# Kernel optimization log

Hardware: AMD Instinct MI355X
Metric: run time of the kernel (lower is better)

Reference implementation:

```python
import jax, jax.numpy as jnp
import numpy as np

D_MODEL = 1440; D_INNER = 2880; D_STATE = 128; HEADDIM = 64; NHEADS = 45
D_CONV = 4; NLAYERS = 32; VOCAB = 256; CHUNK = 128
D_XBC = D_INNER + 2 * D_STATE          # 3136 conv channels
D_PROJ = 2 * D_INNER + 2 * D_STATE + NHEADS  # 6061 in_proj width
EPS = 1e-5

def silu(x):
    return x * jax.nn.sigmoid(x)

def segsum(x):
    # x: (..., T) -> (..., T, T); out[i, j] = sum_{j < k <= i} x[k], -inf above diagonal
    T = x.shape[-1]
    xe = jnp.broadcast_to(x[..., None], (*x.shape, T))
    lower = jnp.tril(jnp.ones((T, T), bool), -1)
    cs = jnp.cumsum(jnp.where(lower, xe, 0.0), axis=-2)
    return jnp.where(jnp.tril(jnp.ones((T, T), bool)), cs, -jnp.inf)

def ssd(X, A, B, C):
    # Chunked SSD (Mamba2 'ssd_minimal_discrete'). X:(b,l,h,p) pre-multiplied by dt,
    # A:(b,l,h) = dt * A_head, B/C:(b,l,n) (ngroups=1, shared across heads).
    b, l, h, p = X.shape
    n = B.shape[-1]
    c = l // CHUNK
    Xc = X.reshape(b, c, CHUNK, h, p)
    Ac = A.reshape(b, c, CHUNK, h).transpose(0, 3, 1, 2)      # (b,h,c,q)
    Bc = B.reshape(b, c, CHUNK, n)
    Cc = C.reshape(b, c, CHUNK, n)
    A_cs = jnp.cumsum(Ac, axis=-1)                            # (b,h,c,q)
    L = jnp.exp(segsum(Ac))                                   # (b,h,c,q,q) intra-chunk decay
    Y_diag = jnp.einsum('bcln,bcsn,bhcls,bcshp->bclhp', Cc, Bc, L, Xc)
    decay_states = jnp.exp(A_cs[..., -1:] - A_cs)             # (b,h,c,q)
    states = jnp.einsum('bcln,bhcl,bclhp->bchpn', Bc, decay_states, Xc)
    A_last = jnp.pad(A_cs[..., -1], ((0, 0), (0, 0), (1, 0)))  # (b,h,c+1)
    decay_chunk = jnp.exp(segsum(A_last))                     # (b,h,c+1,c+1)
    states = jnp.concatenate([jnp.zeros_like(states[:, :1]), states], axis=1)
    states = jnp.einsum('bhzc,bchpn->bzhpn', decay_chunk, states)[:, :-1]  # (b,c,h,p,n)
    Y_off = jnp.einsum('bcln,bchpn,bhcl->bclhp', Cc, states, jnp.exp(A_cs))
    return (Y_diag + Y_off).reshape(b, l, h, p)

def mamba2_block(h, p):
    Win, conv_w, conv_b, dt_bias, A_log, Dp, norm_w, Wout = p
    b, l, _ = h.shape
    zxbcdt = h @ Win                                           # (b,l,6061)
    z = zxbcdt[..., :D_INNER]
    xBC = zxbcdt[..., D_INNER:D_INNER + D_XBC]
    dt = jax.nn.softplus(zxbcdt[..., -NHEADS:] + dt_bias)      # (b,l,H)
    # causal depthwise conv over time, kernel 4
    xp = jnp.pad(xBC, ((0, 0), (D_CONV - 1, 0), (0, 0))).transpose(0, 2, 1)  # (b,C,l+3)
    xBC = jax.lax.conv_general_dilated(xp, conv_w[:, None, :], (1,), 'VALID',
            feature_group_count=D_XBC, dimension_numbers=('NCH', 'OIH', 'NCH'))
    xBC = silu(xBC.transpose(0, 2, 1) + conv_b)                # (b,l,3136)
    x = xBC[..., :D_INNER].reshape(b, l, NHEADS, HEADDIM)
    B = xBC[..., D_INNER:D_INNER + D_STATE]
    C = xBC[..., D_INNER + D_STATE:]
    A = -jnp.exp(A_log)                                        # (H,)
    y = ssd(x * dt[..., None], dt * A, B, C)
    y = y + x * Dp[None, None, :, None]                        # D skip (on raw x)
    y = y.reshape(b, l, D_INNER) * silu(z)                     # gate, then RMSNormGated
    y = y * jax.lax.rsqrt(jnp.mean(y * y, -1, keepdims=True) + EPS) * norm_w
    return y @ Wout

def setup_inputs() -> dict:
    key = jax.random.key(0)
    ks = jax.random.split(key, 8)
    b, l = 2, 2048
    def nrm(k, shape, s=0.02):
        return jax.random.normal(k, shape, jnp.float32) * s
    tokens = jax.random.randint(ks[0], (b, l), 0, VOCAB)
    embed = nrm(ks[1], (VOCAB, D_MODEL))
    Win = nrm(ks[2], (NLAYERS, D_MODEL, D_PROJ))
    conv_w = nrm(ks[3], (NLAYERS, D_XBC, D_CONV), 0.2)
    conv_b = jnp.zeros((NLAYERS, D_XBC), jnp.float32)
    dtv = jnp.exp(jax.random.uniform(ks[4], (NLAYERS, NHEADS)) * (np.log(0.1) - np.log(1e-3)) + np.log(1e-3))
    dt_bias = dtv + jnp.log(-jnp.expm1(-dtv))                  # inverse softplus
    A_log = jnp.log(jax.random.uniform(ks[5], (NLAYERS, NHEADS), minval=1.0, maxval=16.0))
    Dp = jnp.ones((NLAYERS, NHEADS), jnp.float32)
    norm_w = jnp.ones((NLAYERS, D_INNER), jnp.float32)
    Wout = nrm(ks[6], (NLAYERS, D_INNER, D_MODEL))
    final_norm_w = jnp.ones((D_MODEL,), jnp.float32)
    return {'tokens': tokens, 'embed': embed, 'Win': Win, 'conv_w': conv_w,
            'conv_b': conv_b, 'dt_bias': dt_bias, 'A_log': A_log, 'Dp': Dp,
            'norm_w': norm_w, 'Wout': Wout, 'final_norm_w': final_norm_w}

def reference(tokens, embed, Win, conv_w, conv_b, dt_bias, A_log, Dp, norm_w, Wout, final_norm_w):
    h = embed[tokens]                                          # (b,l,d)
    layer_params = (Win, conv_w, conv_b, dt_bias, A_log, Dp, norm_w, Wout)
    def step(carry, p):
        return carry + mamba2_block(carry, p), None
    h, _ = jax.lax.scan(jax.checkpoint(step), h, layer_params)
    h = h * jax.lax.rsqrt(jnp.mean(h * h, -1, keepdims=True) + EPS) * final_norm_w
    return h @ embed.T                                         # tied head -> (b,l,256)
```

## Files before the change

kernel.cpp:

```cpp
#include <hip/hip_runtime.h>
#include <hip/hip_bf16.h>
#include <math.h>

#define NLAYERS 32
#define DM 1440
#define DI 2880
#define DSTATE 128
#define HD 64
#define NH 45
#define VOCABSZ 256
#define CHUNK 128
#define DXBC 3136
#define DPROJ 6061
#define BB 2
#define LL 2048
#define ROWS (BB*LL)
#define NCH (LL/CHUNK)
#define ZXS 6144
#define STR 136
#define STR2 68

typedef __attribute__((ext_vector_type(8))) short bf16x8;
typedef __attribute__((ext_vector_type(4))) float f32x4;
typedef unsigned short us;

__device__ __forceinline__ float sigmoidf_(float x){ return 1.0f/(1.0f+__expf(-x)); }
__device__ __forceinline__ us f2b(float f){
  unsigned int u = __float_as_uint(f);
  return (us)((u + 0x7FFFu + ((u>>16)&1u)) >> 16);
}
__device__ __forceinline__ float b2f(us s){
  return __uint_as_float(((unsigned int)s)<<16);
}
__device__ __forceinline__ void split2(float v, us* ph, us* pl){
  us h = f2b(v);
  *ph = h;
  *pl = f2b(v - b2f(h));
}
__device__ __forceinline__ void gl2lds16(const us* g, us* l){
  __builtin_amdgcn_global_load_lds((const __attribute__((address_space(1))) unsigned int*)g,
                                   (__attribute__((address_space(3))) unsigned int*)l, 16, 0, 0);
}
#define MFMA(a,b,c) __builtin_amdgcn_mfma_f32_16x16x32_bf16(a,b,c,0,0,0)

__global__ void k_embed(const int* __restrict__ tok, const float* __restrict__ emb, float* __restrict__ h){
  int idx = blockIdx.x*256 + threadIdx.x;
  if (idx >= ROWS*DM) return;
  int row = idx / DM, d = idx - row*DM;
  h[idx] = emb[tok[row]*DM + d];
}

__global__ void k_split_rows(const float* __restrict__ src, us* __restrict__ dh,
                             us* __restrict__ dl, int ncols){
  size_t e = ((size_t)blockIdx.x*256 + threadIdx.x)*8;
  const float* s = src + e;
  bf16x8 oh, ol;
  #pragma unroll
  for (int j=0;j<8;j++){
    float v = s[j];
    us hh = f2b(v);
    ((us*)&oh)[j] = hh;
    ((us*)&ol)[j] = f2b(v - b2f(hh));
  }
  *(bf16x8*)(dh + e) = oh;
  *(bf16x8*)(dl + e) = ol;
}

__global__ void k_transcast_sp(const float* __restrict__ W, us* __restrict__ WTh,
                               us* __restrict__ WTl, int K, int N){
  __shared__ float t[32][65];
  int tid = threadIdx.x;
  int n0 = blockIdx.x*64, k0 = blockIdx.y*32;
  #pragma unroll
  for (int i=0;i<8;i++){
    int e = i*256 + tid;
    int r = e >> 6, cc = e & 63;
    int n = n0 + cc;
    t[r][cc] = (n < N) ? W[(size_t)(k0+r)*N + n] : 0.f;
  }
  __syncthreads();
  int nrow = tid >> 2, kseg = (tid & 3)*8;
  bf16x8 oh, ol;
  #pragma unroll
  for (int j=0;j<8;j++){
    float v = t[kseg+j][nrow];
    us hh = f2b(v);
    ((us*)&oh)[j] = hh;
    ((us*)&ol)[j] = f2b(v - b2f(hh));
  }
  *(bf16x8*)(WTh + (size_t)(n0+nrow)*K + k0 + kseg) = oh;
  *(bf16x8*)(WTl + (size_t)(n0+nrow)*K + k0 + kseg) = ol;
}

template<bool ACC, bool SPL>
__global__ __launch_bounds__(256) void k_gemm_sp(const us* __restrict__ Ah, const us* __restrict__ Al,
      const us* __restrict__ Bh, const us* __restrict__ Bl, float* __restrict__ C,
      int K, int ldc, int N, int nbx, us* __restrict__ Oh, us* __restrict__ Ol){
  __shared__ __align__(16) us sAh[4096], sAl[4096], sBh[4096], sBl[4096];
  int nwg = gridDim.x;
  int q = nwg >> 3;
  int bid = blockIdx.x;
  int wg = (bid & 7)*q + (bid >> 3);
  int grp = wg / (4*nbx);
  int rem = wg - grp*4*nbx;
  int by = grp*4 + (rem & 3);
  int bx = rem >> 2;
  int m0 = by*128, n0 = bx*128;
  int tid = threadIdx.x;
  int lane = tid & 63, wid = tid >> 6;
  int wr = wid >> 1, wc = wid & 1;
  int r4 = lane >> 2, c4 = (lane & 3)*8;
  int fr = lane & 15, fk = (lane >> 4)*8;
  f32x4 acc[4][4];
  #pragma unroll
  for (int i=0;i<4;i++)
    #pragma unroll
    for (int j=0;j<4;j++) acc[i][j] = (f32x4){0.f,0.f,0.f,0.f};
  for (int kt = 0; kt < K; kt += 32){
    __syncthreads();
    size_t ra0 = (size_t)(m0 + wid*16     + r4)*K + kt + c4;
    size_t ra1 = (size_t)(m0 + (wid+4)*16 + r4)*K + kt + c4;
    size_t rb0 = (size_t)(n0 + wid*16     + r4)*K + kt + c4;
    size_t rb1 = (size_t)(n0 + (wid+4)*16 + r4)*K + kt + c4;
    gl2lds16(Ah + ra0, sAh + wid*512);
    gl2lds16(Ah + ra1, sAh + (wid+4)*512);
    gl2lds16(Al + ra0, sAl + wid*512);
    gl2lds16(Al + ra1, sAl + (wid+4)*512);
    gl2lds16(Bh + rb0, sBh + wid*512);
    gl2lds16(Bh + rb1, sBh + (wid+4)*512);
    gl2lds16(Bl + rb0, sBl + wid*512);
    gl2lds16(Bl + rb1, sBl + (wid+4)*512);
    __syncthreads();
    bf16x8 ah[4], al[4], bh[4], bl[4];
    #pragma unroll
    for (int i=0;i<4;i++){
      int ro = (wr*64 + i*16 + fr)*32 + fk;
      int co = (wc*64 + i*16 + fr)*32 + fk;
      ah[i] = *(const bf16x8*)(sAh + ro);
      al[i] = *(const bf16x8*)(sAl + ro);
      bh[i] = *(const bf16x8*)(sBh + co);
      bl[i] = *(const bf16x8*)(sBl + co);
    }
    #pragma unroll
    for (int i=0;i<4;i++)
      #pragma unroll
      for (int j=0;j<4;j++){
        acc[i][j] = MFMA(ah[i], bh[j], acc[i][j]);
        acc[i][j] = MFMA(ah[i], bl[j], acc[i][j]);
        acc[i][j] = MFMA(al[i], bh[j], acc[i][j]);
      }
  }
  int orow = (lane>>4)*4, ocol = lane & 15;
  #pragma unroll
  for (int i=0;i<4;i++)
    #pragma unroll
    for (int j=0;j<4;j++)
      #pragma unroll
      for (int r=0;r<4;r++){
        int col = n0 + wc*64 + j*16 + ocol;
        if (col < N){
          size_t off = (size_t)(m0 + wr*64 + i*16 + orow + r)*ldc + col;
          float v = acc[i][j][r] + (ACC ? C[off] : 0.f);
          C[off] = v;
          if (SPL) split2(v, &Oh[off], &Ol[off]);
        }
      }
}

__global__ __launch_bounds__(256) void k_conv2(const float* __restrict__ zx, const float* __restrict__ cw,
                        const float* __restrict__ cb, us* __restrict__ xbh, us* __restrict__ xbl,
                        const float* __restrict__ dtb_in, float* __restrict__ dtb){
  int ch = blockIdx.x*256 + threadIdx.x;
  int l0 = blockIdx.y * 128;
  int b = blockIdx.z;
  if (ch < DXBC){
    float w0 = cw[ch*4+0], w1 = cw[ch*4+1], w2 = cw[ch*4+2], w3 = cw[ch*4+3];
    float bias = cb[ch];
    float x0=0.f, x1=0.f, x2=0.f;
    if (l0-3 >= 0) x0 = zx[(size_t)(b*LL + l0-3)*ZXS + DI + ch];
    if (l0-2 >= 0) x1 = zx[(size_t)(b*LL + l0-2)*ZXS + DI + ch];
    if (l0-1 >= 0) x2 = zx[(size_t)(b*LL + l0-1)*ZXS + DI + ch];
    for (int l = l0; l < l0+128; ++l){
      float x3 = zx[(size_t)(b*LL + l)*ZXS + DI + ch];
      float s = bias + w0*x0 + w1*x1 + w2*x2 + w3*x3;
      float v = s * sigmoidf_(s);
      size_t off = (size_t)(b*LL + l)*DXBC + ch;
      split2(v, &xbh[off], &xbl[off]);
      x0 = x1; x1 = x2; x2 = x3;
    }
  } else if (ch < DXBC + NH){
    int hh = ch - DXBC;
    float bias = dtb_in[hh];
    for (int l = l0; l < l0+128; ++l){
      size_t row = (size_t)(b*LL + l);
      float v = zx[row*ZXS + (DI+DXBC) + hh] + bias;
      dtb[row*NH + hh] = (v > 20.f) ? v : log1pf(__expf(v));
    }
  }
}

__global__ __launch_bounds__(256) void k_sraw(const us* __restrict__ xbh, const us* __restrict__ xbl,
                                              float* __restrict__ Sraw){
  __shared__ __align__(16) us sCh[128*STR], sCl[128*STR], sB2h[128*STR], sB2l[128*STR];
  int tid = threadIdx.x;
  int c = blockIdx.x, b = blockIdx.y;
  int t0 = b*LL + c*CHUNK;
  #pragma unroll
  for (int i=0;i<8;i++){
    int e = i*256 + tid;
    int l = e >> 4, seg = (e & 15)*8;
    size_t oc = (size_t)(t0+l)*DXBC + DI + DSTATE + seg;
    size_t ob = (size_t)(t0+l)*DXBC + DI + seg;
    *(bf16x8*)(sCh + l*STR + seg) = *(const bf16x8*)(xbh + oc);
    *(bf16x8*)(sCl + l*STR + seg) = *(const bf16x8*)(xbl + oc);
    *(bf16x8*)(sB2h + l*STR + seg) = *(const bf16x8*)(xbh + ob);
    *(bf16x8*)(sB2l + l*STR + seg) = *(const bf16x8*)(xbl + ob);
  }
  __syncthreads();
  int lane = tid & 63, wid = tid >> 6;
  int wbase = wid*32;
  int fr = lane & 15, fk = (lane>>4)*8;
  int orow = (lane>>4)*4;
  f32x4 accS[2][8];
  #pragma unroll
  for (int m=0;m<2;m++)
    #pragma unroll
    for (int j=0;j<8;j++) accS[m][j] = (f32x4){0.f,0.f,0.f,0.f};
  #pragma unroll
  for (int ks=0; ks<4; ++ks){
    int ko = ks*32 + fk;
    bf16x8 a0h = *(const bf16x8*)(sCh + (wbase+fr)*STR + ko);
    bf16x8 a0l = *(const bf16x8*)(sCl + (wbase+fr)*STR + ko);
    bf16x8 a1h = *(const bf16x8*)(sCh + (wbase+16+fr)*STR + ko);
    bf16x8 a1l = *(const bf16x8*)(sCl + (wbase+16+fr)*STR + ko);
    #pragma unroll
    for (int j=0;j<8;j++){
      bf16x8 bh = *(const bf16x8*)(sB2h + (j*16+fr)*STR + ko);
      bf16x8 bl = *(const bf16x8*)(sB2l + (j*16+fr)*STR + ko);
      accS[0][j] = MFMA(a0h, bh, accS[0][j]);
      accS[0][j] = MFMA(a0h, bl, accS[0][j]);
      accS[0][j] = MFMA(a0l, bh, accS[0][j]);
      accS[1][j] = MFMA(a1h, bh, accS[1][j]);
      accS[1][j] = MFMA(a1h, bl, accS[1][j]);
      accS[1][j] = MFMA(a1l, bh, accS[1][j]);
    }
  }
  size_t sbase = ((size_t)(b*NCH + c))*16384;
  #pragma unroll
  for (int m=0;m<2;m++)
    #pragma unroll
    for (int j=0;j<8;j++)
      #pragma unroll
      for (int r=0;r<4;r++){
        int l = wbase + m*16 + orow + r;
        int s = j*16 + fr;
        Sraw[sbase + l*128 + s] = accS[m][j][r];
      }
}

__global__ __launch_bounds__(256) void k_ssd_state_sp(const us* __restrict__ xbh, const us* __restrict__ xbl,
    const float* __restrict__ dtb, const float* __restrict__ Alog,
    float* __restrict__ acs, us* __restrict__ cst_h, us* __restrict__ cst_l){
  __shared__ __align__(16) us sBTh[64*STR], sBTl[64*STR];
  __shared__ __align__(16) us sXTh[64*STR], sXTl[64*STR];
  __shared__ float sAcs[128];
  __shared__ float sDt[128];
  int tid = threadIdx.x;
  int hh = blockIdx.x, c = blockIdx.y, b = blockIdx.z;
  int t0 = b*LL + c*CHUNK;
  float A_h = -__expf(Alog[hh]);
  if (tid < 128){
    float d = dtb[(size_t)(t0+tid)*NH + hh];
    sDt[tid] = d;
    sAcs[tid] = d * A_h;
  }
  __syncthreads();
  if (tid < 64){
    float v = sAcs[tid], w = sAcs[64+tid];
    #pragma unroll
    for (int off=1; off<64; off<<=1){
      float tv = __shfl_up(v, off, 64);
      float tw = __shfl_up(w, off, 64);
      if (tid >= off){ v += tv; w += tw; }
    }
    float tot = __shfl(v, 63, 64);
    sAcs[tid] = v;
    sAcs[64+tid] = w + tot;
  }
  __syncthreads();
  if (tid < 128) acs[(size_t)(t0+tid)*NH + hh] = sAcs[tid];
  float alast = sAcs[127];
  #pragma unroll 8
  for (int i=0;i<32;i++){
    int e = i*256 + tid;
    int l = e >> 6, p = e & 63;
    size_t off = (size_t)(t0+l)*DXBC + hh*HD + p;
    float v = (b2f(xbh[off]) + b2f(xbl[off])) * sDt[l] * __expf(alast - sAcs[l]);
    split2(v, &sXTh[p*STR+l], &sXTl[p*STR+l]);
  }
  int lane = tid & 63, wid = tid >> 6;
  int fr = lane & 15, fk = (lane>>4)*8;
  f32x4 acc[8];
  #pragma unroll
  for (int j=0;j<8;j++) acc[j] = (f32x4){0.f,0.f,0.f,0.f};
  #pragma unroll
  for (int nh=0; nh<2; ++nh){
    __syncthreads();
    #pragma unroll 8
    for (int i=0;i<32;i++){
      int e = i*256 + tid;
      int l = e >> 6, n = e & 63;
      size_t off = (size_t)(t0+l)*DXBC + DI + nh*64 + n;
      sBTh[n*STR+l] = xbh[off];
      sBTl[n*STR+l] = xbl[off];
    }
    __syncthreads();
    #pragma unroll
    for (int ks=0; ks<4; ks++){
      bf16x8 ah = *(const bf16x8*)(sXTh + (wid*16 + fr)*STR + ks*32 + fk);
      bf16x8 al = *(const bf16x8*)(sXTl + (wid*16 + fr)*STR + ks*32 + fk);
      #pragma unroll
      for (int j=0;j<4;j++){
        bf16x8 bh = *(const bf16x8*)(sBTh + (j*16 + fr)*STR + ks*32 + fk);
        bf16x8 bl = *(const bf16x8*)(sBTl + (j*16 + fr)*STR + ks*32 + fk);
        acc[nh*4+j] = MFMA(ah, bh, acc[nh*4+j]);
        acc[nh*4+j] = MFMA(ah, bl, acc[nh*4+j]);
        acc[nh*4+j] = MFMA(al, bh, acc[nh*4+j]);
      }
    }
  }
  size_t cbase = (((size_t)(b*NCH + c)*NH) + hh)*8192;
  int orow = (lane>>4)*4;
  #pragma unroll
  for (int jj=0;jj<8;jj++)
    #pragma unroll
    for (int r=0;r<4;r++){
      int p = wid*16 + orow + r;
      int n = (jj>>2)*64 + (jj&3)*16 + fr;
      split2(acc[jj][r], &cst_h[cbase + p*128 + n], &cst_l[cbase + p*128 + n]);
    }
}

__global__ __launch_bounds__(256) void k_ssd_scan2(const float* __restrict__ acs,
      us* __restrict__ cst_h, us* __restrict__ cst_l){
  int tid = threadIdx.x;
  int hh = blockIdx.x, b = blockIdx.y, z = blockIdx.z;
  int base_e = z*1024;
  float P[4];
  #pragma unroll
  for (int i=0;i<4;i++) P[i] = 0.f;
  for (int c=0;c<NCH;c++){
    size_t base = (((size_t)(b*NCH + c)*NH) + hh)*8192 + base_e;
    float dec = __expf(acs[(size_t)(b*LL + c*CHUNK + CHUNK-1)*NH + hh]);
    #pragma unroll
    for (int i=0;i<4;i++){
      size_t e = base + i*256 + tid;
      float tmp = b2f(cst_h[e]) + b2f(cst_l[e]);
      split2(P[i], &cst_h[e], &cst_l[e]);
      P[i] = dec*P[i] + tmp;
    }
  }
}

__global__ __launch_bounds__(512) void k_ssd_y_sp(const us* __restrict__ xbh, const us* __restrict__ xbl,
    const float* __restrict__ dtb, const float* __restrict__ acs,
    const us* __restrict__ cst_h, const us* __restrict__ cst_l,
    const float* __restrict__ Sraw, float* __restrict__ Yf){
  __shared__ __align__(16) us smem[26112];
  __shared__ float sAcs[128];
  __shared__ float sDt[128];
  us* sCh = smem;          us* sCl = smem + 8704;
  us* sPh = smem + 17408;  us* sPl = smem + 21760;
  us* sSh = smem;          us* sSl = smem + 8704;
  us* sXh = smem + 17408;  us* sXl = smem + 21760;

  int tid = threadIdx.x;
  int hh = blockIdx.x, c = blockIdx.y, b = blockIdx.z;
  int t0 = b*LL + c*CHUNK;
  if (tid < 128){
    sAcs[tid] = acs[(size_t)(t0+tid)*NH + hh];
    sDt[tid]  = dtb[(size_t)(t0+tid)*NH + hh];
  }
  int lane = tid & 63, wid = tid >> 6;
  int wbase = wid*16;
  int fr = lane & 15, fk = (lane>>4)*8;
  int orow = (lane>>4)*4;
  size_t cbase = (((size_t)(b*NCH + c)*NH) + hh)*8192;
  size_t sbase = ((size_t)(b*NCH + c))*16384;

  f32x4 accU[4], accD[4];
  #pragma unroll
  for (int j=0;j<4;j++){
    accU[j] = (f32x4){0.f,0.f,0.f,0.f};
    accD[j] = (f32x4){0.f,0.f,0.f,0.f};
  }
  #pragma unroll
  for (int nt=0; nt<2; ++nt){
    int nb = nt*64;
    __syncthreads();
    #pragma unroll 8
    for (int i=0;i<16;i++){
      int e = i*512 + tid;
      int l = e >> 6, nn = e & 63;
      size_t oc = (size_t)(t0+l)*DXBC + DI + DSTATE + nb + nn;
      sCh[l*STR2+nn] = xbh[oc];  sCl[l*STR2+nn] = xbl[oc];
    }
    #pragma unroll 8
    for (int i=0;i<8;i++){
      int e = i*512 + tid;
      int p = e >> 6, nn = e & 63;
      sPh[p*STR2+nn] = cst_h[cbase + p*128 + nb + nn];
      sPl[p*STR2+nn] = cst_l[cbase + p*128 + nb + nn];
    }
    __syncthreads();
    #pragma unroll
    for (int ks=0; ks<2; ++ks){
      int ko = ks*32 + fk;
      bf16x8 a0h = *(const bf16x8*)(sCh + (wbase+fr)*STR2 + ko);
      bf16x8 a0l = *(const bf16x8*)(sCl + (wbase+fr)*STR2 + ko);
      #pragma unroll
      for (int j=0;j<4;j++){
        bf16x8 ph = *(const bf16x8*)(sPh + (j*16+fr)*STR2 + ko);
        bf16x8 pl = *(const bf16x8*)(sPl + (j*16+fr)*STR2 + ko);
        accU[j] = MFMA(a0h, ph, accU[j]);
        accU[j] = MFMA(a0h, pl, accU[j]);
        accU[j] = MFMA(a0l, ph, accU[j]);
      }
    }
  }
  #pragma unroll
  for (int sh=0; sh<2; ++sh){
    __syncthreads();
    #pragma unroll 8
    for (int i=0;i<16;i++){
      int e = i*512 + tid;
      int l = e >> 6, ss = e & 63;
      int s = sh*64 + ss;
      float raw = Sraw[sbase + l*128 + s];
      float v = (s <= l) ? raw*__expf(sAcs[l]-sAcs[s])*sDt[s] : 0.f;
      split2(v, &sSh[l*STR2+ss], &sSl[l*STR2+ss]);
    }
    #pragma unroll 8
    for (int i=0;i<8;i++){
      int e = i*512 + tid;
      int sl = e >> 6, p = e & 63;
      size_t off = (size_t)(t0 + sh*64 + sl)*DXBC + hh*HD + p;
      sXh[p*STR2 + sl] = xbh[off];
      sXl[p*STR2 + sl] = xbl[off];
    }
    __syncthreads();
    #pragma unroll
    for (int ks=0; ks<2; ++ks){
      int ko = ks*32 + fk;
      bf16x8 a0h = *(const bf16x8*)(sSh + (wbase+fr)*STR2 + ko);
      bf16x8 a0l = *(const bf16x8*)(sSl + (wbase+fr)*STR2 + ko);
      #pragma unroll
      for (int j=0;j<4;j++){
        bf16x8 xh = *(const bf16x8*)(sXh + (j*16+fr)*STR2 + ko);
        bf16x8 xl = *(const bf16x8*)(sXl + (j*16+fr)*STR2 + ko);
        accD[j] = MFMA(a0h, xh, accD[j]);
        accD[j] = MFMA(a0h, xl, accD[j]);
        accD[j] = MFMA(a0l, xh, accD[j]);
      }
    }
  }
  #pragma unroll
  for (int r=0;r<4;r++){
    int l = wbase + orow + r;
    float ea = __expf(sAcs[l]);
    #pragma unroll
    for (int j=0;j<4;j++)
      Yf[(size_t)(t0+l)*DI + hh*HD + j*16 + fr] = accD[j][r] + ea*accU[j][r];
  }
}

__global__ __launch_bounds__(256) void k_gatenorm(const float* __restrict__ Yf,
                           const us* __restrict__ xbh, const us* __restrict__ xbl,
                           const float* __restrict__ zx, const float* __restrict__ Dp_l,
                           const float* __restrict__ nw, us* __restrict__ yh, us* __restrict__ yl){
  __shared__ float red[4];
  __shared__ float stot;
  int row = blockIdx.x;
  int tid = threadIdx.x;
  float yv_[12];
  float ss = 0.f;
  #pragma unroll
  for (int i=0;i<12;i++){
    int d = tid + i*256;
    if (d < DI){
      size_t xo = (size_t)row*DXBC + d;
      float xv = b2f(xbh[xo]) + b2f(xbl[xo]);
      float yv = Yf[(size_t)row*DI + d] + xv * Dp_l[d >> 6];
      float zv = zx[(size_t)row*ZXS + d];
      yv *= zv * sigmoidf_(zv);
      yv_[i] = yv;
      ss += yv*yv;
    } else yv_[i] = 0.f;
  }
  #pragma unroll
  for (int off=32; off>0; off>>=1) ss += __shfl_down(ss, off, 64);
  int lane = tid & 63, wid = tid >> 6;
  if (lane == 0) red[wid] = ss;
  __syncthreads();
  if (tid == 0) stot = red[0]+red[1]+red[2]+red[3];
  __syncthreads();
  float rs = rsqrtf(stot / (float)DI + 1e-5f);
  #pragma unroll
  for (int i=0;i<12;i++){
    int d = tid + i*256;
    if (d < DI){
      float v = yv_[i] * rs * nw[d];
      split2(v, &yh[(size_t)row*DI + d], &yl[(size_t)row*DI + d]);
    }
  }
}

__global__ __launch_bounds__(256) void k_finalnorm(const float* __restrict__ h, const float* __restrict__ fnw,
                            us* __restrict__ oh, us* __restrict__ ol){
  __shared__ float red[4];
  __shared__ float stot;
  int row = blockIdx.x;
  int tid = threadIdx.x;
  float v_[6];
  float ss = 0.f;
  #pragma unroll
  for (int i=0;i<6;i++){
    int d = tid + i*256;
    if (d < DM){ v_[i] = h[(size_t)row*DM + d]; ss += v_[i]*v_[i]; }
    else v_[i] = 0.f;
  }
  #pragma unroll
  for (int off=32; off>0; off>>=1) ss += __shfl_down(ss, off, 64);
  int lane = tid & 63, wid = tid >> 6;
  if (lane == 0) red[wid] = ss;
  __syncthreads();
  if (tid == 0) stot = red[0]+red[1]+red[2]+red[3];
  __syncthreads();
  float rs = rsqrtf(stot / (float)DM + 1e-5f);
  #pragma unroll
  for (int i=0;i<6;i++){
    int d = tid + i*256;
    if (d < DM){
      float v = v_[i] * rs * fnw[d];
      split2(v, &oh[(size_t)row*DM + d], &ol[(size_t)row*DM + d]);
    }
  }
}

extern "C" void kernel_launch(void* const* d_in, const int* in_sizes, int n_in,
                              void* d_out, int out_size, void* d_ws, size_t ws_size,
                              hipStream_t stream){
  const int*   tok   = (const int*)d_in[0];
  const float* emb   = (const float*)d_in[1];
  const float* Win   = (const float*)d_in[2];
  const float* convw = (const float*)d_in[3];
  const float* convb = (const float*)d_in[4];
  const float* dtbias= (const float*)d_in[5];
  const float* Alog  = (const float*)d_in[6];
  const float* Dp    = (const float*)d_in[7];
  const float* normw = (const float*)d_in[8];
  const float* Wout  = (const float*)d_in[9];
  const float* fnw   = (const float*)d_in[10];

  float* ws = (float*)d_ws;
  float* h    = ws;
  float* zx   = ws + 5898240;
  us*    xbh  = (us*)(ws + 31064064);
  us*    xbl  = (us*)(ws + 37486592);
  us*    hp_h = (us*)(ws + 31064064);
  us*    hp_l = (us*)(ws + 34013184);
  float* dtb  = ws + 43909120;
  float* acs  = ws + 44093440;
  float* Yf   = ws + 44277760;
  us* wbuf_h  = (us*)(ws + 44277760);
  us* wbuf_l  = (us*)(ws + 48701440);
  us* cst_h   = (us*)(ws + 56074240);
  us* cst_l   = (us*)(ws + 61972480);
  us* ab_h    = (us*)(ws + 56074240);
  us* ab_l    = (us*)(ws + 61972480);
  float* Sraw = ws + 67870720;

  k_embed<<<(ROWS*DM+255)/256, 256, 0, stream>>>(tok, emb, h);
  k_split_rows<<<2880, 256, 0, stream>>>(h, hp_h, hp_l, DM);
  for (int lyr=0; lyr<NLAYERS; ++lyr){
    k_transcast_sp<<<dim3(ZXS/64, DM/32), 256, 0, stream>>>(Win + (size_t)lyr*DM*DPROJ, wbuf_h, wbuf_l, DM, DPROJ);
    k_gemm_sp<false,false><<<(ZXS/128)*(ROWS/128), 256, 0, stream>>>(hp_h, hp_l, wbuf_h, wbuf_l, zx, DM, ZXS, ZXS, ZXS/128, nullptr, nullptr);
    k_conv2<<<dim3(13, 16, BB), 256, 0, stream>>>(
        zx, convw + (size_t)lyr*DXBC*4, convb + (size_t)lyr*DXBC, xbh, xbl,
        dtbias + lyr*NH, dtb);
    k_sraw<<<dim3(NCH, BB), 256, 0, stream>>>(xbh, xbl, Sraw);
    k_ssd_state_sp<<<dim3(NH, NCH, BB), 256, 0, stream>>>(xbh, xbl, dtb, Alog + lyr*NH, acs, cst_h, cst_l);
    k_ssd_scan2<<<dim3(NH, BB, 8), 256, 0, stream>>>(acs, cst_h, cst_l);
    k_ssd_y_sp<<<dim3(NH, NCH, BB), 512, 0, stream>>>(xbh, xbl, dtb, acs, cst_h, cst_l, Sraw, Yf);
    k_gatenorm<<<ROWS, 256, 0, stream>>>(Yf, xbh, xbl, zx, Dp + lyr*NH, normw + (size_t)lyr*DI, ab_h, ab_l);
    k_transcast_sp<<<dim3(1536/64, DI/32), 256, 0, stream>>>(Wout + (size_t)lyr*DI*DM, wbuf_h, wbuf_l, DI, DM);
    k_gemm_sp<true,true><<<(1536/128)*(ROWS/128), 256, 0, stream>>>(ab_h, ab_l, wbuf_h, wbuf_l, h, DI, DM, DM, 1536/128, hp_h, hp_l);
  }
  k_finalnorm<<<ROWS, 256, 0, stream>>>(h, fnw, ab_h, ab_l);
  k_split_rows<<<180, 256, 0, stream>>>(emb, wbuf_h, wbuf_l, DM);
  k_gemm_sp<false,false><<<(VOCABSZ/128)*(ROWS/128), 256, 0, stream>>>(ab_h, ab_l, wbuf_h, wbuf_l, (float*)d_out, DM, VOCABSZ, VOCABSZ, VOCABSZ/128, nullptr, nullptr);
}
```

Baseline: 23.32 ms.

## Load SSD Y operands directly to registers and split conv over more blocks

The SSD output kernel no longer stages C and chunk-state tiles through shared memory. It reads the bf16x8 fragments straight from global memory into MFMA registers and builds the decayed score fragments in registers. X is loaded once into a transposed shared tile, which removes several barriers and most of the LDS traffic. Separately, the conv kernel processes 16 rows per block instead of 128, launching eight times more blocks for better occupancy at the cost of re-reading halo rows.

```diff
diff --git a/kernel.cpp b/kernel.cpp
--- a/kernel.cpp
+++ b/kernel.cpp
@@ -171,7 +171,7 @@
                         const float* __restrict__ cb, us* __restrict__ xbh, us* __restrict__ xbl,
                         const float* __restrict__ dtb_in, float* __restrict__ dtb){
   int ch = blockIdx.x*256 + threadIdx.x;
-  int l0 = blockIdx.y * 128;
+  int l0 = blockIdx.y * 16;
   int b = blockIdx.z;
   if (ch < DXBC){
     float w0 = cw[ch*4+0], w1 = cw[ch*4+1], w2 = cw[ch*4+2], w3 = cw[ch*4+3];
@@ -180,7 +180,8 @@
     if (l0-3 >= 0) x0 = zx[(size_t)(b*LL + l0-3)*ZXS + DI + ch];
     if (l0-2 >= 0) x1 = zx[(size_t)(b*LL + l0-2)*ZXS + DI + ch];
     if (l0-1 >= 0) x2 = zx[(size_t)(b*LL + l0-1)*ZXS + DI + ch];
-    for (int l = l0; l < l0+128; ++l){
+    #pragma unroll 4
+    for (int l = l0; l < l0+16; ++l){
       float x3 = zx[(size_t)(b*LL + l)*ZXS + DI + ch];
       float s = bias + w0*x0 + w1*x1 + w2*x2 + w3*x3;
       float v = s * sigmoidf_(s);
@@ -191,7 +192,8 @@
   } else if (ch < DXBC + NH){
     int hh = ch - DXBC;
     float bias = dtb_in[hh];
-    for (int l = l0; l < l0+128; ++l){
+    #pragma unroll 4
+    for (int l = l0; l < l0+16; ++l){
       size_t row = (size_t)(b*LL + l);
       float v = zx[row*ZXS + (DI+DXBC) + hh] + bias;
       dtb[row*NH + hh] = (v > 20.f) ? v : log1pf(__expf(v));
@@ -366,14 +368,9 @@
     const float* __restrict__ dtb, const float* __restrict__ acs,
     const us* __restrict__ cst_h, const us* __restrict__ cst_l,
     const float* __restrict__ Sraw, float* __restrict__ Yf){
-  __shared__ __align__(16) us smem[26112];
+  __shared__ __align__(16) us sXh[64*STR], sXl[64*STR];
   __shared__ float sAcs[128];
   __shared__ float sDt[128];
-  us* sCh = smem;          us* sCl = smem + 8704;
-  us* sPh = smem + 17408;  us* sPl = smem + 21760;
-  us* sSh = smem;          us* sSl = smem + 8704;
-  us* sXh = smem + 17408;  us* sXl = smem + 21760;
-
   int tid = threadIdx.x;
   int hh = blockIdx.x, c = blockIdx.y, b = blockIdx.z;
   int t0 = b*LL + c*CHUNK;
@@ -381,12 +378,24 @@
     sAcs[tid] = acs[(size_t)(t0+tid)*NH + hh];
     sDt[tid]  = dtb[(size_t)(t0+tid)*NH + hh];
   }
+  #pragma unroll 8
+  for (int i=0;i<16;i++){
+    int e = i*512 + tid;
+    int s = e >> 6, p = e & 63;
+    size_t off = (size_t)(t0+s)*DXBC + hh*HD + p;
+    sXh[p*STR + s] = xbh[off];
+    sXl[p*STR + s] = xbl[off];
+  }
+  __syncthreads();
   int lane = tid & 63, wid = tid >> 6;
   int wbase = wid*16;
   int fr = lane & 15, fk = (lane>>4)*8;
   int orow = (lane>>4)*4;
+  int l = wbase + fr;
+  float acs_l = sAcs[l];
   size_t cbase = (((size_t)(b*NCH + c)*NH) + hh)*8192;
   size_t sbase = ((size_t)(b*NCH + c))*16384;
+  size_t crow  = (size_t)(t0+l)*DXBC + DI + DSTATE;
 
   f32x4 accU[4], accD[4];
   #pragma unroll
@@ -395,82 +404,49 @@
     accD[j] = (f32x4){0.f,0.f,0.f,0.f};
   }
   #pragma unroll
-  for (int nt=0; nt<2; ++nt){
-    int nb = nt*64;
-    __syncthreads();
-    #pragma unroll 8
-    for (int i=0;i<16;i++){
-      int e = i*512 + tid;
-      int l = e >> 6, nn = e & 63;
-      size_t oc = (size_t)(t0+l)*DXBC + DI + DSTATE + nb + nn;
-      sCh[l*STR2+nn] = xbh[oc];  sCl[l*STR2+nn] = xbl[oc];
-    }
-    #pragma unroll 8
-    for (int i=0;i<8;i++){
-      int e = i*512 + tid;
-      int p = e >> 6, nn = e & 63;
-      sPh[p*STR2+nn] = cst_h[cbase + p*128 + nb + nn];
-      sPl[p*STR2+nn] = cst_l[cbase + p*128 + nb + nn];
-    }
-    __syncthreads();
-    #pragma unroll
-    for (int ks=0; ks<2; ++ks){
-      int ko = ks*32 + fk;
-      bf16x8 a0h = *(const bf16x8*)(sCh + (wbase+fr)*STR2 + ko);
-      bf16x8 a0l = *(const bf16x8*)(sCl + (wbase+fr)*STR2 + ko);
-      #pragma unroll
-      for (int j=0;j<4;j++){
-        bf16x8 ph = *(const bf16x8*)(sPh + (j*16+fr)*STR2 + ko);
-        bf16x8 pl = *(const bf16x8*)(sPl + (j*16+fr)*STR2 + ko);
-        accU[j] = MFMA(a0h, ph, accU[j]);
-        accU[j] = MFMA(a0h, pl, accU[j]);
-        accU[j] = MFMA(a0l, ph, accU[j]);
-      }
-    }
-  }
-  #pragma unroll
-  for (int sh=0; sh<2; ++sh){
-    __syncthreads();
-    #pragma unroll 8
-    for (int i=0;i<16;i++){
-      int e = i*512 + tid;
-      int l = e >> 6, ss = e & 63;
-      int s = sh*64 + ss;
-      float raw = Sraw[sbase + l*128 + s];
-      float v = (s <= l) ? raw*__expf(sAcs[l]-sAcs[s])*sDt[s] : 0.f;
-      split2(v, &sSh[l*STR2+ss], &sSl[l*STR2+ss]);
-    }
-    #pragma unroll 8
-    for (int i=0;i<8;i++){
-      int e = i*512 + tid;
-      int sl = e >> 6, p = e & 63;
-      size_t off = (size_t)(t0 + sh*64 + sl)*DXBC + hh*HD + p;
-      sXh[p*STR2 + sl] = xbh[off];
-      sXl[p*STR2 + sl] = xbl[off];
-    }
-    __syncthreads();
-    #pragma unroll
-    for (int ks=0; ks<2; ++ks){
-      int ko = ks*32 + fk;
-      bf16x8 a0h = *(const bf16x8*)(sSh + (wbase+fr)*STR2 + ko);
-      bf16x8 a0l = *(const bf16x8*)(sSl + (wbase+fr)*STR2 + ko);
-      #pragma unroll
-      for (int j=0;j<4;j++){
-        bf16x8 xh = *(const bf16x8*)(sXh + (j*16+fr)*STR2 + ko);
-        bf16x8 xl = *(const bf16x8*)(sXl + (j*16+fr)*STR2 + ko);
-        accD[j] = MFMA(a0h, xh, accD[j]);
-        accD[j] = MFMA(a0h, xl, accD[j]);
-        accD[j] = MFMA(a0l, xh, accD[j]);
-      }
+  for (int kk=0; kk<4; ++kk){
+    int ko = kk*32 + fk;
+    bf16x8 ch8 = *(const bf16x8*)(xbh + crow + ko);
+    bf16x8 cl8 = *(const bf16x8*)(xbl + crow + ko);
+    #pragma unroll
+    for (int j=0;j<4;j++){
+      int prow = j*16 + fr;
+      bf16x8 ph = *(const bf16x8*)(cst_h + cbase + prow*128 + ko);
+      bf16x8 pl = *(const bf16x8*)(cst_l + cbase + prow*128 + ko);
+      accU[j] = MFMA(ch8, ph, accU[j]);
+      accU[j] = MFMA(ch8, pl, accU[j]);
+      accU[j] = MFMA(cl8, ph, accU[j]);
+    }
+  }
+  #pragma unroll
+  for (int kk=0; kk<4; ++kk){
+    int sc = kk*32 + fk;
+    const float* rp = Sraw + sbase + (size_t)l*128 + sc;
+    bf16x8 ah, al;
+    #pragma unroll
+    for (int jj=0;jj<8;jj++){
+      int s = sc + jj;
+      float v = (s <= l) ? rp[jj]*__expf(acs_l - sAcs[s])*sDt[s] : 0.f;
+      us h2 = f2b(v);
+      ((us*)&ah)[jj] = h2;
+      ((us*)&al)[jj] = f2b(v - b2f(h2));
+    }
+    #pragma unroll
+    for (int j=0;j<4;j++){
+      bf16x8 xh = *(const bf16x8*)(sXh + (j*16+fr)*STR + sc);
+      bf16x8 xl = *(const bf16x8*)(sXl + (j*16+fr)*STR + sc);
+      accD[j] = MFMA(ah, xh, accD[j]);
+      accD[j] = MFMA(ah, xl, accD[j]);
+      accD[j] = MFMA(al, xh, accD[j]);
     }
   }
   #pragma unroll
   for (int r=0;r<4;r++){
-    int l = wbase + orow + r;
-    float ea = __expf(sAcs[l]);
+    int lo = wbase + orow + r;
+    float ea = __expf(sAcs[lo]);
     #pragma unroll
     for (int j=0;j<4;j++)
-      Yf[(size_t)(t0+l)*DI + hh*HD + j*16 + fr] = accD[j][r] + ea*accU[j][r];
+      Yf[(size_t)(t0+lo)*DI + hh*HD + j*16 + fr] = accD[j][r] + ea*accU[j][r];
   }
 }
 
@@ -585,7 +561,7 @@
   for (int lyr=0; lyr<NLAYERS; ++lyr){
     k_transcast_sp<<<dim3(ZXS/64, DM/32), 256, 0, stream>>>(Win + (size_t)lyr*DM*DPROJ, wbuf_h, wbuf_l, DM, DPROJ);
     k_gemm_sp<false,false><<<(ZXS/128)*(ROWS/128), 256, 0, stream>>>(hp_h, hp_l, wbuf_h, wbuf_l, zx, DM, ZXS, ZXS, ZXS/128, nullptr, nullptr);
-    k_conv2<<<dim3(13, 16, BB), 256, 0, stream>>>(
+    k_conv2<<<dim3(13, 128, BB), 256, 0, stream>>>(
         zx, convw + (size_t)lyr*DXBC*4, convb + (size_t)lyr*DXBC, xbh, xbl,
         dtbias + lyr*NH, dtb);
     k_sraw<<<dim3(NCH, BB), 256, 0, stream>>>(xbh, xbl, Sraw);
```

New measurement: 19.63 ms. 15.8% less time.
